# Kernel optimization log

Measured on AMD Instinct MI355X. Metric: run time of the kernel, lower is better.

## Reference

```python
import jax, jax.numpy as jnp
import numpy as np

B, L, C = 8, 16384, 128
H, WS, SHIFT = 4, 64, 32
NW = L // WS
HD = C // H
HID = 4 * C
SCALE = HD ** -0.5
EPS = 1e-5


def _build_mask():
    # standard Swin cyclic-shift attention mask (1D)
    img_mask = np.zeros((1, L, 1), dtype=np.float32)
    cnt = 0
    for sl in (slice(0, -WS), slice(-WS, -SHIFT), slice(-SHIFT, None)):
        img_mask[:, sl, :] = cnt
        cnt += 1
    mw = img_mask.reshape(1, NW, WS)[0]            # (nW, WS)
    attn_mask = mw[:, None, :] - mw[:, :, None]    # (nW, WS, WS)
    attn_mask = np.where(attn_mask != 0, -100.0, 0.0).astype(np.float32)
    return jnp.asarray(attn_mask)


def setup_inputs() -> dict:
    key = jax.random.key(0)
    ks = jax.random.split(key, 12)
    s = 0.02
    return {
        'x': jax.random.normal(ks[0], (B, L, C), jnp.float32),
        'mask': _build_mask(),
        'gamma1': jnp.ones((C,), jnp.float32),
        'beta1': jnp.zeros((C,), jnp.float32),
        'w_qkv': jax.random.normal(ks[1], (C, 3 * C), jnp.float32) * s,
        'b_qkv': jnp.zeros((3 * C,), jnp.float32),
        'rel_bias': jax.random.normal(ks[2], (2 * WS - 1, H), jnp.float32) * s,
        'w_proj': jax.random.normal(ks[3], (C, C), jnp.float32) * s,
        'b_proj': jnp.zeros((C,), jnp.float32),
        'gamma2': jnp.ones((C,), jnp.float32),
        'beta2': jnp.zeros((C,), jnp.float32),
        'w_fc1': jax.random.normal(ks[4], (C, HID), jnp.float32) * s,
        'b_fc1': jnp.zeros((HID,), jnp.float32),
        'w_fc2': jax.random.normal(ks[5], (HID, C), jnp.float32) * s,
        'b_fc2': jnp.zeros((C,), jnp.float32),
    }


def _ln(x, g, b):
    m = jnp.mean(x, -1, keepdims=True)
    v = jnp.mean((x - m) ** 2, -1, keepdims=True)
    return (x - m) * jax.lax.rsqrt(v + EPS) * g + b


def reference(x, mask, gamma1, beta1, w_qkv, b_qkv, rel_bias, w_proj, b_proj,
              gamma2, beta2, w_fc1, b_fc1, w_fc2, b_fc2):
    shortcut = x
    h = _ln(x, gamma1, beta1)
    # cyclic shift (L % WS == 0 so no padding needed)
    h = jnp.roll(h, -SHIFT, axis=1)
    # window partition -> (B*nW, WS, C)
    hw = h.reshape(B * NW, WS, C)
    qkv = hw @ w_qkv + b_qkv                                  # (Bw, WS, 3C)
    qkv = qkv.reshape(B * NW, WS, 3, H, HD).transpose(2, 0, 3, 1, 4)
    q, k, v = qkv[0] * SCALE, qkv[1], qkv[2]                  # (Bw, H, WS, HD)
    attn = jnp.einsum('whqd,whkd->whqk', q, k)                # (Bw, H, WS, WS)
    # relative position bias
    idx = jnp.arange(WS)[:, None] - jnp.arange(WS)[None, :] + WS - 1  # (WS, WS)
    bias = rel_bias[idx].transpose(2, 0, 1)                   # (H, WS, WS)
    attn = attn + bias[None]
    # shift mask per window
    attn = attn.reshape(B, NW, H, WS, WS) + mask[None, :, None]
    attn = jax.nn.softmax(attn, axis=-1).reshape(B * NW, H, WS, WS)
    out = jnp.einsum('whqk,whkd->whqd', attn, v)              # (Bw, H, WS, HD)
    out = out.transpose(0, 2, 1, 3).reshape(B * NW, WS, C)
    out = out @ w_proj + b_proj
    # window reverse + reverse shift
    out = out.reshape(B, L, C)
    out = jnp.roll(out, SHIFT, axis=1)
    x1 = shortcut + out
    # MLP (exact GELU, as torch nn.GELU default)
    m = _ln(x1, gamma2, beta2)
    m = jax.nn.gelu(m @ w_fc1 + b_fc1, approximate=False) @ w_fc2 + b_fc2
    return x1 + m
```

## Files before the change

kernel.cpp:

```cpp
#include <hip/hip_runtime.h>
#include <math.h>

#define B_ 8
#define L_ 16384
#define C_ 128
#define H_ 4
#define WS_ 64
#define SHIFT_ 32
#define NW_ 256
#define HD_ 32
#define HID_ 512
#define M_ (B_*L_)
#define SCALE_ 0.17677669529663687f
#define EPS_ 1e-5f

using short8 = __attribute__((ext_vector_type(8))) short;
using f32x4  = __attribute__((ext_vector_type(4))) float;
using gas1   = const __attribute__((address_space(1))) unsigned int*;
using las3   = __attribute__((address_space(3))) unsigned int*;
typedef unsigned short ushort_t;

#define GLDS(GP, LP) __builtin_amdgcn_global_load_lds((gas1)(const void*)(GP), \
                                                      (las3)(void*)(LP), 16, 0, 0)

__device__ __forceinline__ f32x4 mfma16(short8 a, short8 b, f32x4 c) {
    return __builtin_amdgcn_mfma_f32_16x16x32_bf16(a, b, c, 0, 0, 0);
}

__device__ __forceinline__ ushort_t f2bf(float v)
{
    unsigned u = __float_as_uint(v);
    return (ushort_t)((u + 0x7fff + ((u >> 16) & 1)) >> 16);
}
__device__ __forceinline__ void bsplit(float v, ushort_t& h, ushort_t& l)
{
    unsigned b = __float_as_uint(v);
    h = (ushort_t)(b >> 16);
    float vh = __uint_as_float(b & 0xffff0000u);
    l = (ushort_t)(__float_as_uint(v - vh) >> 16);
}
__device__ __forceinline__ float bf2f(unsigned s) { return __uint_as_float(s << 16); }

__device__ __forceinline__ float gelu_f(float x)
{
    float u = 1.5957691216057308f * (x + 0.044715f * x * x * x);
    float e = __expf(u);
    float t = 1.f - 2.f / (e + 1.f);
    return 0.5f * x * (1.f + t);
}

__global__ __launch_bounds__(256)
void ln_ts(const float* __restrict__ in, ushort_t* __restrict__ oh,
           ushort_t* __restrict__ ol,
           const float* __restrict__ gamma, const float* __restrict__ beta,
           int do_shift, int m_off)
{
    int m    = blockIdx.x * 4 + (threadIdx.x >> 6);
    int lane = threadIdx.x & 63;
    int gr   = m_off + m;
    int src  = gr;
    if (do_shift) {
        int b = gr >> 14, l = gr & (L_ - 1);
        src = (b << 14) | ((l + SHIFT_) & (L_ - 1));
    }
    const float* row = in + (size_t)src * C_;
    float2 v = *(const float2*)&row[lane * 2];
    float s  = v.x + v.y;
    float ss = v.x * v.x + v.y * v.y;
#pragma unroll
    for (int off = 1; off < 64; off <<= 1) {
        s  += __shfl_xor(s, off);
        ss += __shfl_xor(ss, off);
    }
    float mean = s * (1.f / C_);
    float var  = ss * (1.f / C_) - mean * mean;
    float rstd = rsqrtf(var + EPS_);
    float2 g  = *(const float2*)&gamma[lane * 2];
    float2 bt = *(const float2*)&beta[lane * 2];
    float ox = (v.x - mean) * rstd * g.x + bt.x;
    float oy = (v.y - mean) * rstd * g.y + bt.y;
    int k = lane * 2;
    unsigned idx = (unsigned)((m >> 4) * 16 + (k >> 3)) * 128 + (m & 15) * 8 + (k & 7);
    ushort_t h0, l0, h1, l1;
    bsplit(ox, h0, l0); bsplit(oy, h1, l1);
    *(unsigned*)&oh[idx] = (unsigned)h0 | ((unsigned)h1 << 16);
    *(unsigned*)&ol[idx] = (unsigned)l0 | ((unsigned)l1 << 16);
}

__global__ __launch_bounds__(256)
void wconv(const float* __restrict__ wq, const float* __restrict__ wp,
           const float* __restrict__ w1, const float* __restrict__ w2,
           ushort_t* __restrict__ th)
{
    int e = blockIdx.x * 256 + threadIdx.x;
    const float* W; int K, N, base, local;
    if (e < 49152)       { W = wq; K = 128; N = 384; base = 0;      local = e; }
    else if (e < 65536)  { W = wp; K = 128; N = 128; base = 49152;  local = e - 49152; }
    else if (e < 131072) { W = w1; K = 128; N = 512; base = 65536;  local = e - 65536; }
    else                 { W = w2; K = 512; N = 128; base = 131072; local = e - 131072; }
    int n = local / K, k = local % K;
    int idx = base + ((n >> 4) * (K >> 3) + (k >> 3)) * 128 + (n & 15) * 8 + (k & 7);
    th[idx] = f2bf(W[(size_t)k * N + n]);
}

__global__ __launch_bounds__(256)
void attn_kernel(const ushort_t* __restrict__ qkv, const float* __restrict__ relb,
                 ushort_t* __restrict__ Oh, ushort_t* __restrict__ Ol,
                 int w_off)
{
    __shared__ ushort_t SH[24576];
    __shared__ float bls[H_][128];
    const int w    = blockIdx.x;
    const int h    = threadIdx.x >> 6;
    const int lane = threadIdx.x & 63;
    ushort_t* QP = SH + h * 4096;
    ushort_t* VT = SH + 16384 + h * 2048;

    const ushort_t* base = qkv + (size_t)w * WS_ * 384 + h * HD_;

    bls[h][lane] = relb[lane * H_ + h];
    if (lane < 63) bls[h][lane + 64] = relb[(lane + 64) * H_ + h];

#pragma unroll
    for (int it = 0; it < 4; ++it) {
        int f = it * 64 + lane;
        int r = f >> 2, oct = f & 3;
        uint4 vq = *(const uint4*)&base[r * 384 + oct * 8];
        uint4 vk = *(const uint4*)&base[r * 384 + C_ + oct * 8];
        int ti = ((r >> 4) * 4 + oct) * 128 + (r & 15) * 8;
        *(uint4*)&QP[ti]        = vq;
        *(uint4*)&QP[2048 + ti] = vk;
    }
#pragma unroll
    for (int it = 0; it < 4; ++it) {
        int f = it * 64 + lane;
        int r = f >> 2, oct = f & 3;
        ushort_t tmp[8];
        *(uint4*)tmp = *(const uint4*)&base[r * 384 + 2 * C_ + oct * 8];
#pragma unroll
        for (int e = 0; e < 8; ++e) {
            int d = oct * 8 + e;
            VT[((d >> 4) * 8 + (r >> 3)) * 128 + (d & 15) * 8 + (r & 7)] = tmp[e];
        }
    }

    f32x4 acc[4][4];
    {
        const int lro = (lane >> 4) * 128 + (lane & 15) * 8;
        short8 aq[4], bk[4];
#pragma unroll
        for (int i = 0; i < 4; ++i) aq[i] = *(const short8*)&QP[i * 512 + lro];
#pragma unroll
        for (int j = 0; j < 4; ++j) bk[j] = *(const short8*)&QP[2048 + j * 512 + lro];
        const f32x4 z = {0.f, 0.f, 0.f, 0.f};
#pragma unroll
        for (int i = 0; i < 4; ++i)
#pragma unroll
        for (int j = 0; j < 4; ++j)
            acc[i][j] = mfma16(aq[i], bk[j], z);
    }

    const int wn = (w_off + w) & (NW_ - 1);
    const bool lastw = (wn == NW_ - 1);
#pragma unroll
    for (int i = 0; i < 4; ++i)
#pragma unroll
    for (int j = 0; j < 4; ++j) {
        const int bidx = i * 16 + (lane >> 4) * 4 - j * 16 - (lane & 15) + 63;
        const float mv = (lastw && ((i ^ j) & 2)) ? -100.f : 0.f;
#pragma unroll
        for (int r = 0; r < 4; ++r)
            acc[i][j][r] = acc[i][j][r] * SCALE_ + bls[h][bidx + r] + mv;
    }
    float mx[4][4], sm[4][4];
#pragma unroll
    for (int i = 0; i < 4; ++i)
#pragma unroll
    for (int r = 0; r < 4; ++r) {
        float m = fmaxf(fmaxf(acc[i][0][r], acc[i][1][r]),
                        fmaxf(acc[i][2][r], acc[i][3][r]));
#pragma unroll
        for (int off = 1; off < 16; off <<= 1) m = fmaxf(m, __shfl_xor(m, off));
        mx[i][r] = m;
    }
#pragma unroll
    for (int i = 0; i < 4; ++i)
#pragma unroll
    for (int j = 0; j < 4; ++j)
#pragma unroll
    for (int r = 0; r < 4; ++r)
        acc[i][j][r] = __expf(acc[i][j][r] - mx[i][r]);
#pragma unroll
    for (int i = 0; i < 4; ++i)
#pragma unroll
    for (int r = 0; r < 4; ++r) {
        float s = acc[i][0][r] + acc[i][1][r] + acc[i][2][r] + acc[i][3][r];
#pragma unroll
        for (int off = 1; off < 16; off <<= 1) s += __shfl_xor(s, off);
        sm[i][r] = 1.f / s;
    }
#pragma unroll
    for (int i = 0; i < 4; ++i)
#pragma unroll
    for (int j = 0; j < 4; ++j) {
        const int kb   = j * 2 + ((lane & 15) >> 3);
        const int koff = lane & 7;
#pragma unroll
        for (int r = 0; r < 4; ++r)
            QP[(i * 8 + kb) * 128 + ((lane >> 4) * 4 + r) * 8 + koff] =
                f2bf(acc[i][j][r] * sm[i][r]);
    }
    f32x4 oacc[4][2] = {};
    {
        short8 vb[2][2];
#pragma unroll
        for (int dp = 0; dp < 2; ++dp)
#pragma unroll
        for (int kk = 0; kk < 2; ++kk)
            vb[dp][kk] = *(const short8*)&VT[(dp * 8 + kk * 4 + (lane >> 4)) * 128 + (lane & 15) * 8];
#pragma unroll
        for (int i = 0; i < 4; ++i)
#pragma unroll
        for (int kk = 0; kk < 2; ++kk) {
            short8 pa = *(const short8*)&QP[(i * 8 + kk * 4 + (lane >> 4)) * 128 + (lane & 15) * 8];
#pragma unroll
            for (int dp = 0; dp < 2; ++dp)
                oacc[i][dp] = mfma16(pa, vb[dp][kk], oacc[i][dp]);
        }
    }
    const int gm0 = w * WS_;
#pragma unroll
    for (int i = 0; i < 4; ++i)
#pragma unroll
    for (int dp = 0; dp < 2; ++dp) {
        const int c  = h * HD_ + dp * 16 + (lane & 15);
        const int cb = c >> 3;
#pragma unroll
        for (int r = 0; r < 4; ++r) {
            const int gm = gm0 + i * 16 + (lane >> 4) * 4 + r;
            const size_t idx = ((size_t)(gm >> 4) * 16 + cb) * 128 + (gm & 15) * 8 + (c & 7);
            ushort_t hh, ll; bsplit(oacc[i][dp][r], hh, ll);
            Oh[idx] = hh; Ol[idx] = ll;
        }
    }
}

template<int EPI>
__global__ __launch_bounds__(256, 2)
void mgemm(const ushort_t* __restrict__ Ahi, const ushort_t* __restrict__ Alo,
           const ushort_t* __restrict__ Bhi,
           const float* __restrict__ bias, float* __restrict__ Cd,
           ushort_t* __restrict__ Cb, const float* __restrict__ X,
           int M, int N, int K, int m_off)
{
    __shared__ ushort_t lds[2][3][4096];
    const int t    = threadIdx.x;
    const int lane = t & 63, wid = t >> 6;
    const int wmP  = (wid >> 1) * 4;
    const int wnP  = (wid & 1) * 4;
    const int pm0  = blockIdx.x * 8;
    const int pn0  = blockIdx.y * 8;
    const int lro  = (lane >> 4) * 128 + (lane & 15) * 8;
    const size_t pstr = (size_t)16 * K;

    f32x4 acc[4][4] = {};

#define STAGE(buf, kc) { \
    const size_t ko = (size_t)((kc) >> 3) * 128; \
    _Pragma("unroll") \
    for (int sh = 0; sh < 2; ++sh) { \
        const int f = sh * 2048 + t * 8; \
        const int p = f >> 9, o = f & 511; \
        const size_t ga = (size_t)(pm0 + p) * pstr + ko + o; \
        const size_t gb = (size_t)(pn0 + p) * pstr + ko + o; \
        GLDS(Ahi + ga, &lds[buf][0][f]); \
        GLDS(Alo + ga, &lds[buf][1][f]); \
        GLDS(Bhi + gb, &lds[buf][2][f]); \
    } }

#define COMPUTE(buf) { \
    short8 ah[4], al[4], bh[4]; \
    _Pragma("unroll") for (int i = 0; i < 4; ++i) { \
        ah[i] = *(const short8*)&lds[buf][0][(wmP + i) * 512 + lro]; \
        al[i] = *(const short8*)&lds[buf][1][(wmP + i) * 512 + lro]; \
        bh[i] = *(const short8*)&lds[buf][2][(wnP + i) * 512 + lro]; \
    } \
    _Pragma("unroll") for (int i = 0; i < 4; ++i) \
    _Pragma("unroll") for (int j = 0; j < 4; ++j) { \
        acc[i][j] = mfma16(ah[i], bh[j], acc[i][j]); \
        acc[i][j] = mfma16(al[i], bh[j], acc[i][j]); \
    } }

    const int nst = K >> 5;
    STAGE(0, 0);
    __syncthreads();
    int cur = 0;
    for (int c = 0; c < nst; ++c) {
        if (c + 1 < nst) STAGE(cur ^ 1, (c + 1) << 5);
        COMPUTE(cur);
        __syncthreads();
        cur ^= 1;
    }
#undef STAGE
#undef COMPUTE

    const int m0r = blockIdx.x * 128;
    const int n0  = blockIdx.y * 128;
#pragma unroll
    for (int j = 0; j < 4; ++j) {
        const int col = n0 + (wid & 1) * 64 + j * 16 + (lane & 15);
        const float bv = bias[col];
#pragma unroll
        for (int i = 0; i < 4; ++i) {
#pragma unroll
            for (int r = 0; r < 4; ++r) {
                const int row = m0r + (wid >> 1) * 64 + i * 16 + (lane >> 4) * 4 + r;
                float v = acc[i][j][r] + bv;
                if (EPI == 0) {
                    Cb[(size_t)row * N + col] = f2bf(v);
                } else {
                    int gr = m_off + row;
                    int b = gr >> 14, l = gr & (L_ - 1);
                    size_t dst = ((size_t)((b << 14) | ((l + SHIFT_) & (L_ - 1)))) * C_ + col;
                    Cd[dst] = v + X[dst];
                }
            }
        }
    }
}

__global__ __launch_bounds__(256, 2)
void mlp_k(const ushort_t* __restrict__ Ahi, const ushort_t* __restrict__ Alo,
           const ushort_t* __restrict__ W1t, const ushort_t* __restrict__ W2t,
           const float* __restrict__ b1, const float* __restrict__ b2,
           float* __restrict__ Out, int m_off)
{
    __shared__ ushort_t Wq[16384];
    __shared__ ushort_t Gs[4][4096];
    const int t = threadIdx.x, lane = t & 63, w = t >> 6;
    const int g = lane >> 4, c = lane & 15;
    const int rp0 = blockIdx.x * 8 + w * 2;
    ushort_t* gs = Gs[w];

#pragma unroll
    for (int it = 0; it < 8; ++it) { int f = it * 2048 + t * 8; GLDS(W1t + f, &Wq[f]); }
    __syncthreads();

    f32x4 acc2[2][8] = {};
    for (int q = 0; q < 4; ++q) {
        f32x4 acc1[2][8] = {};
#pragma unroll
        for (int ks = 0; ks < 4; ++ks) {
            short8 mh[2], ml[2], wf[8];
#pragma unroll
            for (int jb = 0; jb < 2; ++jb) {
                size_t ai = (size_t)(rp0 + jb) * 2048 + (ks * 4 + g) * 128 + c * 8;
                mh[jb] = *(const short8*)&Ahi[ai];
                ml[jb] = *(const short8*)&Alo[ai];
            }
#pragma unroll
            for (int cb = 0; cb < 8; ++cb)
                wf[cb] = *(const short8*)&Wq[cb * 2048 + (ks * 4 + g) * 128 + c * 8];
#pragma unroll
            for (int jb = 0; jb < 2; ++jb)
#pragma unroll
            for (int cb = 0; cb < 8; ++cb) {
                acc1[jb][cb] = mfma16(mh[jb], wf[cb], acc1[jb][cb]);
                acc1[jb][cb] = mfma16(ml[jb], wf[cb], acc1[jb][cb]);
            }
        }
        __syncthreads();
        if (q < 3) {
            const ushort_t* src = W1t + (q + 1) * 16384;
#pragma unroll
            for (int it = 0; it < 8; ++it) { int f = it * 2048 + t * 8; GLDS(src + f, &Wq[f]); }
        }
#pragma unroll
        for (int jb = 0; jb < 2; ++jb)
#pragma unroll
        for (int cb = 0; cb < 8; ++cb) {
            const int kg = cb * 16 + c;
            const float bb = b1[q * 128 + kg];
#pragma unroll
            for (int r = 0; r < 4; ++r) {
                float v = gelu_f(acc1[jb][cb][r] + bb);
                gs[(jb * 16 + (kg >> 3)) * 128 + (g * 4 + r) * 8 + (kg & 7)] = f2bf(v);
            }
        }
#pragma unroll
        for (int ks = 0; ks < 4; ++ks) {
            short8 w2f[8], ga[2];
#pragma unroll
            for (int ocb = 0; ocb < 8; ++ocb) {
                size_t wi = (size_t)ocb * 8192 + (q * 16 + ks * 4 + g) * 128 + c * 8;
                w2f[ocb] = *(const short8*)&W2t[wi];
            }
#pragma unroll
            for (int jb = 0; jb < 2; ++jb)
                ga[jb] = *(const short8*)&gs[(jb * 16 + ks * 4 + g) * 128 + c * 8];
#pragma unroll
            for (int jb = 0; jb < 2; ++jb)
#pragma unroll
            for (int ocb = 0; ocb < 8; ++ocb)
                acc2[jb][ocb] = mfma16(ga[jb], w2f[ocb], acc2[jb][ocb]);
        }
        __syncthreads();
    }
#pragma unroll
    for (int jb = 0; jb < 2; ++jb)
#pragma unroll
    for (int ocb = 0; ocb < 8; ++ocb) {
        const int col = ocb * 16 + c;
        const float bb = b2[col];
#pragma unroll
        for (int r = 0; r < 4; ++r) {
            const int row = blockIdx.x * 128 + w * 32 + jb * 16 + g * 4 + r;
            size_t di = (size_t)(m_off + row) * C_ + col;
            Out[di] += acc2[jb][ocb][r] + bb;
        }
    }
}

extern "C" void kernel_launch(void* const* d_in, const int* in_sizes, int n_in,
                              void* d_out, int out_size, void* d_ws, size_t ws_size,
                              hipStream_t stream)
{
    const float* x      = (const float*)d_in[0];
    const float* gamma1 = (const float*)d_in[2];
    const float* beta1  = (const float*)d_in[3];
    const float* w_qkv  = (const float*)d_in[4];
    const float* b_qkv  = (const float*)d_in[5];
    const float* relb   = (const float*)d_in[6];
    const float* w_proj = (const float*)d_in[7];
    const float* b_proj = (const float*)d_in[8];
    const float* gamma2 = (const float*)d_in[9];
    const float* beta2  = (const float*)d_in[10];
    const float* w_fc1  = (const float*)d_in[11];
    const float* b_fc1  = (const float*)d_in[12];
    const float* w_fc2  = (const float*)d_in[13];
    const float* b_fc2  = (const float*)d_in[14];
    float* out = (float*)d_out;

    int nch = 8;
    for (int c = 1; c <= 8; c <<= 1) {
        size_t need = 393216 + (size_t)(M_ / c) * 1792;
        if (need <= ws_size) { nch = c; break; }
    }
    const int Mc = M_ / nch;

    ushort_t* wth  = (ushort_t*)d_ws;
    ushort_t* dynp = wth + 196608;
    ushort_t* h_hi = dynp;
    ushort_t* h_lo = h_hi + (size_t)Mc * C_;
    ushort_t* a_hi = h_lo + (size_t)Mc * C_;
    ushort_t* a_lo = a_hi + (size_t)Mc * C_;
    ushort_t* qkvb = a_lo + (size_t)Mc * C_;

    wconv<<<dim3(768), dim3(256), 0, stream>>>(w_qkv, w_proj, w_fc1, w_fc2, wth);

    for (int ch = 0; ch < nch; ++ch) {
        int m0 = ch * Mc;

        ln_ts<<<dim3(Mc / 4), dim3(256), 0, stream>>>(x, h_hi, h_lo, gamma1, beta1, 1, m0);

        mgemm<0><<<dim3(Mc / 128, 3), dim3(256), 0, stream>>>(
            h_hi, h_lo, wth, b_qkv, nullptr, qkvb, nullptr, Mc, 3 * C_, C_, 0);

        attn_kernel<<<dim3(Mc / WS_), dim3(256), 0, stream>>>(
            qkvb, relb, a_hi, a_lo, m0 / WS_);

        mgemm<1><<<dim3(Mc / 128, 1), dim3(256), 0, stream>>>(
            a_hi, a_lo, wth + 49152, b_proj, out, nullptr, x, Mc, C_, C_, m0);

        ln_ts<<<dim3(Mc / 4), dim3(256), 0, stream>>>(out, h_hi, h_lo, gamma2, beta2, 0, m0);

        mlp_k<<<dim3(Mc / 128), dim3(256), 0, stream>>>(
            h_hi, h_lo, wth + 65536, wth + 131072, b_fc1, b_fc2, out, m0);
    }
}
```

Baseline: 455.9 us.

## Fuse second LayerNorm into proj GEMM epilogue and stage W2 in LDS

The proj GEMM epilogue now adds bias and residual, computes per-row mean and variance through shuffles and an LDS reduction, and writes the LN2 output as hi/lo bf16 tiles, which removes the separate ln_ts launch and its re-read of the output. The MLP kernel keeps its A fragments in registers across the hidden chunks and stages W2 slices in LDS with async loads, where before they came from global memory. The GELU staging buffer is cut in half so LDS fits. Costs are more registers and LDS, which may lower occupancy, and a one-pass variance formula that is less numerically stable.

New measurement: 452.9 us. No clear change (-0.7%).

```diff
diff --git a/kernel.cpp b/kernel.cpp
--- a/kernel.cpp
+++ b/kernel.cpp
@@ -251,6 +251,8 @@
            const ushort_t* __restrict__ Bhi,
            const float* __restrict__ bias, float* __restrict__ Cd,
            ushort_t* __restrict__ Cb, const float* __restrict__ X,
+           const float* __restrict__ G2, const float* __restrict__ B2,
+           ushort_t* __restrict__ Gh, ushort_t* __restrict__ Gl,
            int M, int N, int K, int m_off)
 {
     __shared__ ushort_t lds[2][3][4096];
@@ -306,24 +308,79 @@
 
     const int m0r = blockIdx.x * 128;
     const int n0  = blockIdx.y * 128;
-#pragma unroll
-    for (int j = 0; j < 4; ++j) {
-        const int col = n0 + (wid & 1) * 64 + j * 16 + (lane & 15);
-        const float bv = bias[col];
-#pragma unroll
-        for (int i = 0; i < 4; ++i) {
+
+    if (EPI == 0) {
+#pragma unroll
+        for (int j = 0; j < 4; ++j) {
+            const int col = n0 + (wid & 1) * 64 + j * 16 + (lane & 15);
+            const float bv = bias[col];
+#pragma unroll
+            for (int i = 0; i < 4; ++i)
 #pragma unroll
             for (int r = 0; r < 4; ++r) {
                 const int row = m0r + (wid >> 1) * 64 + i * 16 + (lane >> 4) * 4 + r;
-                float v = acc[i][j][r] + bv;
-                if (EPI == 0) {
-                    Cb[(size_t)row * N + col] = f2bf(v);
-                } else {
-                    int gr = m_off + row;
-                    int b = gr >> 14, l = gr & (L_ - 1);
-                    size_t dst = ((size_t)((b << 14) | ((l + SHIFT_) & (L_ - 1)))) * C_ + col;
-                    Cd[dst] = v + X[dst];
-                }
+                Cb[(size_t)row * N + col] = f2bf(acc[i][j][r] + bv);
+            }
+        }
+    } else {
+        float* sf = (float*)&lds[0][0][0];
+        float bv[4], g2v[4], b2v[4];
+#pragma unroll
+        for (int j = 0; j < 4; ++j) {
+            const int col = (wid & 1) * 64 + j * 16 + (lane & 15);
+            bv[j] = bias[col]; g2v[j] = G2[col]; b2v[j] = B2[col];
+        }
+#pragma unroll
+        for (int i = 0; i < 4; ++i)
+#pragma unroll
+        for (int r = 0; r < 4; ++r) {
+            const int row = m0r + (wid >> 1) * 64 + i * 16 + (lane >> 4) * 4 + r;
+            const int gr = m_off + row;
+            const int bb = gr >> 14, l = gr & (L_ - 1);
+            const size_t drow = (size_t)((bb << 14) | ((l + SHIFT_) & (L_ - 1)));
+            float s = 0.f, ss = 0.f;
+#pragma unroll
+            for (int j = 0; j < 4; ++j) {
+                const int col = (wid & 1) * 64 + j * 16 + (lane & 15);
+                float v = acc[i][j][r] + bv[j] + X[drow * C_ + col];
+                Cd[drow * C_ + col] = v;
+                acc[i][j][r] = v;
+                s += v; ss += v * v;
+            }
+#pragma unroll
+            for (int off = 1; off < 16; off <<= 1) {
+                s  += __shfl_xor(s, off);
+                ss += __shfl_xor(ss, off);
+            }
+            if ((lane & 15) == 0) {
+                const int rl = (wid >> 1) * 64 + i * 16 + (lane >> 4) * 4 + r;
+                sf[(wid & 1) * 256 + rl * 2 + 0] = s;
+                sf[(wid & 1) * 256 + rl * 2 + 1] = ss;
+            }
+        }
+        __syncthreads();
+#pragma unroll
+        for (int i = 0; i < 4; ++i)
+#pragma unroll
+        for (int r = 0; r < 4; ++r) {
+            const int rl  = (wid >> 1) * 64 + i * 16 + (lane >> 4) * 4 + r;
+            const int row = m0r + rl;
+            const int gr = m_off + row;
+            const int bb = gr >> 14, l = gr & (L_ - 1);
+            const int dloc = ((bb << 14) | ((l + SHIFT_) & (L_ - 1))) - m_off;
+            const float st  = sf[rl * 2 + 0] + sf[256 + rl * 2 + 0];
+            const float sst = sf[rl * 2 + 1] + sf[256 + rl * 2 + 1];
+            const float mean = st * (1.f / C_);
+            const float var  = sst * (1.f / C_) - mean * mean;
+            const float rstd = rsqrtf(var + EPS_);
+#pragma unroll
+            for (int j = 0; j < 4; ++j) {
+                const int col = (wid & 1) * 64 + j * 16 + (lane & 15);
+                const float m2 = (acc[i][j][r] - mean) * rstd * g2v[j] + b2v[j];
+                ushort_t hh, ll; bsplit(m2, hh, ll);
+                const size_t idx = ((size_t)(dloc >> 4) * 16 + (col >> 3)) * 128
+                                 + (dloc & 15) * 8 + (col & 7);
+                Gh[idx] = hh; Gl[idx] = ll;
             }
         }
     }
@@ -336,14 +393,29 @@
            float* __restrict__ Out, int m_off)
 {
     __shared__ ushort_t Wq[16384];
-    __shared__ ushort_t Gs[4][4096];
+    __shared__ ushort_t W2q[16384];
+    __shared__ ushort_t Gs[4][2048];
     const int t = threadIdx.x, lane = t & 63, w = t >> 6;
     const int g = lane >> 4, c = lane & 15;
     const int rp0 = blockIdx.x * 8 + w * 2;
     ushort_t* gs = Gs[w];
 
+    short8 mh[2][4], ml[2][4];
+#pragma unroll
+    for (int jb = 0; jb < 2; ++jb)
+#pragma unroll
+    for (int ks = 0; ks < 4; ++ks) {
+        const size_t ai = (size_t)(rp0 + jb) * 2048 + (ks * 4 + g) * 128 + c * 8;
+        mh[jb][ks] = *(const short8*)&Ahi[ai];
+        ml[jb][ks] = *(const short8*)&Alo[ai];
+    }
 #pragma unroll
     for (int it = 0; it < 8; ++it) { int f = it * 2048 + t * 8; GLDS(W1t + f, &Wq[f]); }
+#pragma unroll
+    for (int it = 0; it < 8; ++it) {
+        int f = it * 2048 + t * 8; int p = f >> 11, o = f & 2047;
+        GLDS(W2t + (size_t)p * 8192 + o, &W2q[f]);
+    }
     __syncthreads();
 
     f32x4 acc2[2][8] = {};
@@ -351,22 +423,14 @@
         f32x4 acc1[2][8] = {};
 #pragma unroll
         for (int ks = 0; ks < 4; ++ks) {
-            short8 mh[2], ml[2], wf[8];
-#pragma unroll
-            for (int jb = 0; jb < 2; ++jb) {
-                size_t ai = (size_t)(rp0 + jb) * 2048 + (ks * 4 + g) * 128 + c * 8;
-                mh[jb] = *(const short8*)&Ahi[ai];
-                ml[jb] = *(const short8*)&Alo[ai];
-            }
-#pragma unroll
-            for (int cb = 0; cb < 8; ++cb)
-                wf[cb] = *(const short8*)&Wq[cb * 2048 + (ks * 4 + g) * 128 + c * 8];
-#pragma unroll
-            for (int jb = 0; jb < 2; ++jb)
 #pragma unroll
             for (int cb = 0; cb < 8; ++cb) {
-                acc1[jb][cb] = mfma16(mh[jb], wf[cb], acc1[jb][cb]);
-                acc1[jb][cb] = mfma16(ml[jb], wf[cb], acc1[jb][cb]);
+                const short8 wf = *(const short8*)&Wq[cb * 2048 + (ks * 4 + g) * 128 + c * 8];
+#pragma unroll
+                for (int jb = 0; jb < 2; ++jb) {
+                    acc1[jb][cb] = mfma16(mh[jb][ks], wf, acc1[jb][cb]);
+                    acc1[jb][cb] = mfma16(ml[jb][ks], wf, acc1[jb][cb]);
+                }
             }
         }
         __syncthreads();
@@ -376,35 +440,44 @@
             for (int it = 0; it < 8; ++it) { int f = it * 2048 + t * 8; GLDS(src + f, &Wq[f]); }
         }
 #pragma unroll
-        for (int jb = 0; jb < 2; ++jb)
-#pragma unroll
-        for (int cb = 0; cb < 8; ++cb) {
-            const int kg = cb * 16 + c;
-            const float bb = b1[q * 128 + kg];
-#pragma unroll
-            for (int r = 0; r < 4; ++r) {
-                float v = gelu_f(acc1[jb][cb][r] + bb);
-                gs[(jb * 16 + (kg >> 3)) * 128 + (g * 4 + r) * 8 + (kg & 7)] = f2bf(v);
-            }
-        }
-#pragma unroll
-        for (int ks = 0; ks < 4; ++ks) {
-            short8 w2f[8], ga[2];
-#pragma unroll
-            for (int ocb = 0; ocb < 8; ++ocb) {
-                size_t wi = (size_t)ocb * 8192 + (q * 16 + ks * 4 + g) * 128 + c * 8;
-                w2f[ocb] = *(const short8*)&W2t[wi];
-            }
+        for (int hh = 0; hh < 2; ++hh) {
 #pragma unroll
             for (int jb = 0; jb < 2; ++jb)
-                ga[jb] = *(const short8*)&gs[(jb * 16 + ks * 4 + g) * 128 + c * 8];
-#pragma unroll
-            for (int jb = 0; jb < 2; ++jb)
-#pragma unroll
-            for (int ocb = 0; ocb < 8; ++ocb)
-                acc2[jb][ocb] = mfma16(ga[jb], w2f[ocb], acc2[jb][ocb]);
+#pragma unroll
+            for (int cb4 = 0; cb4 < 4; ++cb4) {
+                const int cb = hh * 4 + cb4;
+                const int kg = cb4 * 16 + c;
+                const float bb = b1[q * 128 + hh * 64 + kg];
+#pragma unroll
+                for (int r = 0; r < 4; ++r) {
+                    const float v = gelu_f(acc1[jb][cb][r] + bb);
+                    gs[(jb * 8 + (kg >> 3)) * 128 + (g * 4 + r) * 8 + (kg & 7)] = f2bf(v);
+                }
+            }
+#pragma unroll
+            for (int kk = 0; kk < 2; ++kk) {
+                const int ksq = hh * 2 + kk;
+                short8 ga[2];
+#pragma unroll
+                for (int jb = 0; jb < 2; ++jb)
+                    ga[jb] = *(const short8*)&gs[(jb * 8 + kk * 4 + g) * 128 + c * 8];
+#pragma unroll
+                for (int ocb = 0; ocb < 8; ++ocb) {
+                    const short8 w2f = *(const short8*)&W2q[ocb * 2048 + (ksq * 4 + g) * 128 + c * 8];
+#pragma unroll
+                    for (int jb = 0; jb < 2; ++jb)
+                        acc2[jb][ocb] = mfma16(ga[jb], w2f, acc2[jb][ocb]);
+                }
+            }
         }
         __syncthreads();
+        if (q < 3) {
+#pragma unroll
+            for (int it = 0; it < 8; ++it) {
+                int f = it * 2048 + t * 8; int p = f >> 11, o = f & 2047;
+                GLDS(W2t + (size_t)p * 8192 + (q + 1) * 2048 + o, &W2q[f]);
+            }
+        }
     }
 #pragma unroll
     for (int jb = 0; jb < 2; ++jb)
@@ -464,15 +537,15 @@
         ln_ts<<<dim3(Mc / 4), dim3(256), 0, stream>>>(x, h_hi, h_lo, gamma1, beta1, 1, m0);
 
         mgemm<0><<<dim3(Mc / 128, 3), dim3(256), 0, stream>>>(
-            h_hi, h_lo, wth, b_qkv, nullptr, qkvb, nullptr, Mc, 3 * C_, C_, 0);
+            h_hi, h_lo, wth, b_qkv, nullptr, qkvb, nullptr,
+            nullptr, nullptr, nullptr, nullptr, Mc, 3 * C_, C_, 0);
 
         attn_kernel<<<dim3(Mc / WS_), dim3(256), 0, stream>>>(
             qkvb, relb, a_hi, a_lo, m0 / WS_);
 
         mgemm<1><<<dim3(Mc / 128, 1), dim3(256), 0, stream>>>(
-            a_hi, a_lo, wth + 49152, b_proj, out, nullptr, x, Mc, C_, C_, m0);
-
-        ln_ts<<<dim3(Mc / 4), dim3(256), 0, stream>>>(out, h_hi, h_lo, gamma2, beta2, 0, m0);
+            a_hi, a_lo, wth + 49152, b_proj, out, nullptr, x,
+            gamma2, beta2, h_hi, h_lo, Mc, C_, C_, m0);
 
         mlp_k<<<dim3(Mc / 128), dim3(256), 0, stream>>>(
             h_hi, h_lo, wth + 65536, wth + 131072, b_fc1, b_fc2, out, m0);
```
